# Kernel tuning notes

Measured on AMD Instinct MI355X. Metric: run time of the kernel, lower is better.

## Reference

```python
import jax, jax.numpy as jnp
import numpy as np

D = 1024      # in_features
H = 8         # heads per branch (head_num // 2)
DH = (D // 2) // H  # 64
OUT = 1024

def _split_heads(x, B, S):
    # [B, S, D/2] -> [B, H, S, DH]
    return x.reshape(B, S, H, DH).transpose(0, 2, 1, 3)

def _attn(q, k, v):
    # q,k,v: [B, H, S, DH]
    scores = jnp.einsum('bhqd,bhkd->bhqk', q, k) / jnp.sqrt(jnp.float32(DH))
    a = jax.nn.softmax(scores, axis=-1)
    return jnp.einsum('bhqk,bhkd->bhqd', a, v)

def setup_inputs() -> dict:
    key = jax.random.key(0)
    ks = jax.random.split(key, 16)
    B, S = 2, 2048
    d2 = D // 2
    sc = lambda fan_in: 1.0 / np.sqrt(fan_in)
    inp = {
        'f1': jax.random.normal(ks[0], (B, S, D), jnp.float32),
        'f2': jax.random.normal(ks[1], (B, S, D), jnp.float32),
    }
    names = ['qs', 'ks', 'vs', 'qc', 'kc', 'vc']
    for i, n in enumerate(names):
        inp['W' + n] = jax.random.uniform(ks[2 + i], (d2, D), jnp.float32, -sc(D), sc(D))
        inp['b' + n] = jax.random.uniform(ks[8 + i], (d2,), jnp.float32, -sc(D), sc(D))
    inp['Wo'] = jax.random.uniform(ks[14], (OUT, 2 * D), jnp.float32, -sc(2 * D), sc(2 * D))
    inp['bo'] = jax.random.uniform(ks[15], (OUT,), jnp.float32, -sc(2 * D), sc(2 * D))
    return inp

def reference(f1, f2, Wqs, bqs, Wks, bks, Wvs, bvs, Wqc, bqc, Wkc, bkc, Wvc, bvc, Wo, bo):
    B, S, _ = f1.shape
    lin = lambda x, W, b: jax.nn.relu(x @ W.T + b)
    qs = lin(f1, Wqs, bqs); ks_ = lin(f1, Wks, bks); vs = lin(f1, Wvs, bvs)
    qc = lin(f1, Wqc, bqc); kc = lin(f2, Wkc, bkc); vc = lin(f2, Wvc, bvc)
    ys = _attn(_split_heads(qs, B, S), _split_heads(ks_, B, S), _split_heads(vs, B, S))
    yc = _attn(_split_heads(qc, B, S), _split_heads(kc, B, S), _split_heads(vc, B, S))
    merge = lambda y: y.transpose(0, 2, 1, 3).reshape(B, S, D // 2)
    # reshape_to_batches followed by reshape_from_batches on vs/vc is identity
    y = jnp.concatenate([merge(ys), merge(yc), vs, vc], axis=-1)  # [B, S, 2D]
    return jax.nn.relu(y @ Wo.T + bo)
```

## Files before the change

### kernel.cpp

```cpp
#include <hip/hip_runtime.h>
#include <hip/hip_bf16.h>

using bf16 = __hip_bfloat16;
typedef __attribute__((ext_vector_type(8))) short bf16x8;
typedef __attribute__((ext_vector_type(4))) short s16x4;
typedef __attribute__((ext_vector_type(4))) float f32x4;
typedef __attribute__((ext_vector_type(16))) float f32x16;
typedef __attribute__((ext_vector_type(4))) unsigned int u32x4;

#define MTOT 4096

__device__ __forceinline__ f32x4 fzero() {
    f32x4 z = {0.f, 0.f, 0.f, 0.f};
    return z;
}
__device__ __forceinline__ f32x16 fzero16() {
    f32x16 z = {0.f,0.f,0.f,0.f,0.f,0.f,0.f,0.f,0.f,0.f,0.f,0.f,0.f,0.f,0.f,0.f};
    return z;
}

__device__ __forceinline__ f32x4 mfma16(bf16x8 a, bf16x8 b, f32x4 c) {
    return __builtin_amdgcn_mfma_f32_16x16x32_bf16(a, b, c, 0, 0, 0);
}
__device__ __forceinline__ f32x16 mfma32(bf16x8 a, bf16x8 b, f32x16 c) {
    return __builtin_amdgcn_mfma_f32_32x32x16_bf16(a, b, c, 0, 0, 0);
}

__device__ __forceinline__ float exp2_raw(float x) {
    float r;
    asm("v_exp_f32 %0, %1" : "=v"(r) : "v"(x));
    return r;
}

typedef const __attribute__((address_space(1))) unsigned int* gas_ptr;
typedef __attribute__((address_space(3))) unsigned int* las_ptr;
__device__ __forceinline__ void async_copy16(const bf16* g, bf16* l) {
    __builtin_amdgcn_global_load_lds((gas_ptr)(const void*)g, (las_ptr)(void*)l, 16, 0, 0);
}

__device__ __forceinline__ bf16x8 load8(const bf16* p) {
    return *(const bf16x8*)p;
}
__device__ __forceinline__ bf16x8 load8(const float* p) {
    float4 a = *(const float4*)p;
    float4 b = *(const float4*)(p + 4);
    bf16 t[8];
    t[0] = __float2bfloat16(a.x); t[1] = __float2bfloat16(a.y);
    t[2] = __float2bfloat16(a.z); t[3] = __float2bfloat16(a.w);
    t[4] = __float2bfloat16(b.x); t[5] = __float2bfloat16(b.y);
    t[6] = __float2bfloat16(b.z); t[7] = __float2bfloat16(b.w);
    return *(const bf16x8*)t;
}

__device__ __forceinline__ void store_out(bf16* C, size_t idx, float v) {
    C[idx] = __float2bfloat16(v);
}
__device__ __forceinline__ void store_out(float* C, size_t idx, float v) {
    C[idx] = v;
}
__device__ __forceinline__ short bf16_bits(float v) {
    return __builtin_bit_cast(short, __float2bfloat16(v));
}

__global__ void MultiHeadSelfCrossAttention_7834020348638_kernel(float* out, int n) {
    int i = blockIdx.x * blockDim.x + threadIdx.x;
    if (i < n) out[i] = 0.25f;
}

struct CvtArgs {
    const float* src[9];
    bf16* dst[9];
    int start8[10];
};
__global__ void cvt_kernel(CvtArgs a) {
    int t = blockIdx.x * blockDim.x + threadIdx.x;
    if (t >= a.start8[9]) return;
    int seg = 0;
#pragma unroll
    for (int s = 1; s < 9; s++) seg += (t >= a.start8[s]) ? 1 : 0;
    int off = t - a.start8[seg];
    *(bf16x8*)(a.dst[seg] + (size_t)off * 8) = load8(a.src[seg] + (size_t)off * 8);
}

template <int BM, int BN, typename TC>
__device__ __forceinline__ void gemm_fast(
    const bf16* __restrict__ A, int lda,
    const bf16* __restrict__ Bt, int ldb,
    const float* __restrict__ bias,
    TC* __restrict__ C, int ldc,
    int K, int m0, int n0, bf16* __restrict__ VTW)
{
    constexpr int MI  = BM / 32;
    constexpr int NI  = BN / 32;
    constexpr int ACH = BM * 64 / 8 / 256;
    constexpr int BCH = BN * 64 / 8 / 256;

    __shared__ bf16 As[BM * 64];
    __shared__ bf16 Bs[BN * 64];

    const int tid  = threadIdx.x;
    const int lane = tid & 63;
    const int l15  = lane & 15, quad = lane >> 4;
    const int wave = tid >> 6;
    const int wr   = wave >> 1, wc = wave & 1;

    f32x4 acc[MI][NI];
#pragma unroll
    for (int mi = 0; mi < MI; mi++)
#pragma unroll
        for (int ni = 0; ni < NI; ni++)
            acc[mi][ni] = fzero();

    for (int k0 = 0; k0 < K; k0 += 64) {
        __syncthreads();
#pragma unroll
        for (int i = 0; i < ACH; i++) {
            int idx = i * 256 + tid;
            int r   = idx >> 3;
            int sl  = (idx & 7) ^ (r & 7);
            async_copy16(A + (size_t)(m0 + r) * lda + k0 + sl * 8, &As[idx * 8]);
        }
#pragma unroll
        for (int i = 0; i < BCH; i++) {
            int idx = i * 256 + tid;
            int r   = idx >> 3;
            int sl  = (idx & 7) ^ (r & 7);
            async_copy16(Bt + (size_t)(n0 + r) * ldb + k0 + sl * 8, &Bs[idx * 8]);
        }
        __syncthreads();

#pragma unroll
        for (int ks = 0; ks < 2; ks++) {
            bf16x8 af[MI], bfr[NI];
#pragma unroll
            for (int mi = 0; mi < MI; mi++) {
                int row = wr * (BM / 2) + mi * 16 + l15;
                af[mi] = *(const bf16x8*)&As[row * 64 + (((ks * 4 + quad) ^ (row & 7)) * 8)];
            }
#pragma unroll
            for (int ni = 0; ni < NI; ni++) {
                int row = wc * (BN / 2) + ni * 16 + l15;
                bfr[ni] = *(const bf16x8*)&Bs[row * 64 + (((ks * 4 + quad) ^ (row & 7)) * 8)];
            }
#pragma unroll
            for (int mi = 0; mi < MI; mi++)
#pragma unroll
                for (int ni = 0; ni < NI; ni++)
                    acc[mi][ni] = mfma16(af[mi], bfr[ni], acc[mi][ni]);
        }
    }

#pragma unroll
    for (int ni = 0; ni < NI; ni++) {
        int col = n0 + wc * (BN / 2) + ni * 16 + l15;
        float bb = bias[col];
#pragma unroll
        for (int mi = 0; mi < MI; mi++) {
            float v0 = fmaxf(acc[mi][ni][0] + bb, 0.f);
            float v1 = fmaxf(acc[mi][ni][1] + bb, 0.f);
            float v2 = fmaxf(acc[mi][ni][2] + bb, 0.f);
            float v3 = fmaxf(acc[mi][ni][3] + bb, 0.f);
            int row0 = m0 + wr * (BM / 2) + mi * 16 + quad * 4;
            store_out(C, (size_t)(row0 + 0) * ldc + col, v0);
            store_out(C, (size_t)(row0 + 1) * ldc + col, v1);
            store_out(C, (size_t)(row0 + 2) * ldc + col, v2);
            store_out(C, (size_t)(row0 + 3) * ldc + col, v3);
            if (VTW) {
                int h = col >> 6, d = col & 63;
                int s = row0 & 2047, b2 = row0 >> 11;
                short tv[4] = {bf16_bits(v0), bf16_bits(v1), bf16_bits(v2), bf16_bits(v3)};
                *(s16x4*)&VTW[((size_t)(b2 * 8 + h)) * 64 * 2048 + (size_t)d * 2048 + s] =
                    *(const s16x4*)tv;
            }
        }
    }
}

template <int BN, typename TA, typename TB, typename TC>
__device__ __forceinline__ void gemm_reg(
    const TA* __restrict__ A, int lda,
    const TB* __restrict__ Bt, int ldb,
    const float* __restrict__ bias,
    TC* __restrict__ C, int ldc,
    int K, int m0, int n0)
{
    constexpr int NI  = BN / 32;
    constexpr int BCH = BN * 4 / 256;

    __shared__ bf16 As[128 * 32];
    __shared__ bf16 Bs[BN * 32];

    const int tid  = threadIdx.x;
    const int lane = tid & 63;
    const int l15  = lane & 15, quad = lane >> 4;
    const int wave = tid >> 6;
    const int wr   = wave >> 1, wc = wave & 1;

    f32x4 acc[4][NI];
#pragma unroll
    for (int mi = 0; mi < 4; mi++)
#pragma unroll
        for (int ni = 0; ni < NI; ni++)
            acc[mi][ni] = fzero();

    for (int k0 = 0; k0 < K; k0 += 32) {
        bf16x8 ra[2], rb[BCH];
#pragma unroll
        for (int i = 0; i < 2; i++) {
            int idx = i * 256 + tid;
            ra[i] = load8(A + (size_t)(m0 + (idx >> 2)) * lda + k0 + (idx & 3) * 8);
        }
#pragma unroll
        for (int i = 0; i < BCH; i++) {
            int idx = i * 256 + tid;
            rb[i] = load8(Bt + (size_t)(n0 + (idx >> 2)) * ldb + k0 + (idx & 3) * 8);
        }
        __syncthreads();
#pragma unroll
        for (int i = 0; i < 2; i++)
            *(bf16x8*)&As[(i * 256 + tid) * 8] = ra[i];
#pragma unroll
        for (int i = 0; i < BCH; i++)
            *(bf16x8*)&Bs[(i * 256 + tid) * 8] = rb[i];
        __syncthreads();

        bf16x8 af[4], bfr[NI];
#pragma unroll
        for (int mi = 0; mi < 4; mi++)
            af[mi] = *(const bf16x8*)&As[(wr * 64 + mi * 16 + l15) * 32 + quad * 8];
#pragma unroll
        for (int ni = 0; ni < NI; ni++)
            bfr[ni] = *(const bf16x8*)&Bs[(wc * (BN / 2) + ni * 16 + l15) * 32 + quad * 8];
#pragma unroll
        for (int mi = 0; mi < 4; mi++)
#pragma unroll
            for (int ni = 0; ni < NI; ni++)
                acc[mi][ni] = mfma16(af[mi], bfr[ni], acc[mi][ni]);
    }

#pragma unroll
    for (int ni = 0; ni < NI; ni++) {
        int col = n0 + wc * (BN / 2) + ni * 16 + l15;
        float bb = bias[col];
#pragma unroll
        for (int mi = 0; mi < 4; mi++) {
#pragma unroll
            for (int r = 0; r < 4; r++) {
                int row = m0 + wr * 64 + mi * 16 + quad * 4 + r;
                store_out(C, (size_t)row * ldc + col, fmaxf(acc[mi][ni][r] + bb, 0.f));
            }
        }
    }
}

__global__ __launch_bounds__(256, 4) void proj_fast(
    const bf16* __restrict__ F1, const bf16* __restrict__ F2,
    const bf16* __restrict__ Wb,
    const float* __restrict__ bqs, const float* __restrict__ bks,
    const float* __restrict__ bvs, const float* __restrict__ bqc,
    const float* __restrict__ bkc, const float* __restrict__ bvc,
    bf16* __restrict__ Y, bf16* Qs, bf16* Ks, bf16* Qc, bf16* Kc,
    bf16* __restrict__ VT)
{
    const int lid   = blockIdx.x;
    const int xcd   = lid & 7, slot = lid >> 3;
    const int panel = xcd * 24 + (slot >> 2);
    const int xb    = slot & 3;
    const int g     = panel >> 5, yb = panel & 31;
    const int m0 = yb * 128, n0 = xb * 128;

    const bf16* X; const float* bi; bf16* C; int ldc;
    switch (g) {
        case 0:  X = F1; bi = bqs; C = Qs;       ldc = 512;  break;
        case 1:  X = F1; bi = bks; C = Ks;       ldc = 512;  break;
        case 2:  X = F1; bi = bvs; C = Y + 1024; ldc = 2048; break;
        case 3:  X = F1; bi = bqc; C = Qc;       ldc = 512;  break;
        case 4:  X = F2; bi = bkc; C = Kc;       ldc = 512;  break;
        default: X = F2; bi = bvc; C = Y + 1536; ldc = 2048; break;
    }
    bf16* vtw = nullptr;
    if (VT && (g == 2 || g == 5))
        vtw = VT + (size_t)(g == 5 ? 2 * 8 * 64 * 2048 : 0);
    gemm_fast<128, 128, bf16>(X, 1024, Wb + (size_t)g * 512 * 1024, 1024, bi, C, ldc,
                              1024, m0, n0, vtw);
}

__global__ __launch_bounds__(256, 4) void out_fast(
    const bf16* __restrict__ Y, const bf16* __restrict__ WoB,
    const float* __restrict__ bo, float* __restrict__ out)
{
    const int lid   = blockIdx.x;
    const int xcd   = lid & 7, slot = lid >> 3;
    const int panel = xcd * 8 + (slot >> 4);
    const int xb    = slot & 15;
    gemm_fast<64, 64, float>(Y, 2048, WoB, 2048, bo, out, 1024, 2048,
                             panel * 64, xb * 64, nullptr);
}

__global__ void proj_reg(
    const float* __restrict__ f1, const float* __restrict__ f2,
    const float* __restrict__ Wqs, const float* __restrict__ bqs,
    const float* __restrict__ Wks, const float* __restrict__ bks,
    const float* __restrict__ Wvs, const float* __restrict__ bvs,
    const float* __restrict__ Wqc, const float* __restrict__ bqc,
    const float* __restrict__ Wkc, const float* __restrict__ bkc,
    const float* __restrict__ Wvc, const float* __restrict__ bvc,
    bf16* __restrict__ Y, bf16* Qs, bf16* Ks, bf16* Qc, bf16* Kc)
{
    const int g = blockIdx.z;
    const float *X, *W, *bi; bf16* C; int ldc;
    switch (g) {
        case 0:  X = f1; W = Wqs; bi = bqs; C = Qs;       ldc = 512;  break;
        case 1:  X = f1; W = Wks; bi = bks; C = Ks;       ldc = 512;  break;
        case 2:  X = f1; W = Wvs; bi = bvs; C = Y + 1024; ldc = 2048; break;
        case 3:  X = f1; W = Wqc; bi = bqc; C = Qc;       ldc = 512;  break;
        case 4:  X = f2; W = Wkc; bi = bkc; C = Kc;       ldc = 512;  break;
        default: X = f2; W = Wvc; bi = bvc; C = Y + 1536; ldc = 2048; break;
    }
    gemm_reg<128>(X, 1024, W, 1024, bi, C, ldc, 1024, blockIdx.y * 128, blockIdx.x * 128);
}

__global__ void out_reg(const bf16* __restrict__ Y, const float* __restrict__ Wo,
                        const float* __restrict__ bo, float* __restrict__ out)
{
    gemm_reg<64>(Y, 2048, Wo, 2048, bo, out, 1024, 2048, blockIdx.y * 128, blockIdx.x * 64);
}

__global__ __launch_bounds__(256, 4) void attn2_kernel(
    const bf16* __restrict__ Qsb, const bf16* __restrict__ Ksb,
    const bf16* __restrict__ Qcb, const bf16* __restrict__ Kcb,
    const bf16* __restrict__ VT, bf16* __restrict__ Y)
{
    __shared__ bf16 SMEM[4][64 * 64];

    const int tid  = threadIdx.x;
    const int lane = tid & 63;
    const int l31  = lane & 31;
    const int hi   = lane >> 5;
    const int wave = tid >> 6;

    const int lid   = blockIdx.x + 16 * blockIdx.y + 256 * blockIdx.z;
    const int xcd   = lid & 7, slot = lid >> 3;
    const int combo = xcd + 8 * (slot >> 4);
    const int qt    = slot & 15;
    const int bh    = combo & 15, br = combo >> 4;
    const int b = bh >> 3, h = bh & 7;

    const bf16* Qb = (br ? Qcb : Qsb) + (size_t)b * 2048 * 512 + h * 64;
    const bf16* Kb = (br ? Kcb : Ksb) + (size_t)b * 2048 * 512 + h * 64;
    const bf16* Vt = VT + ((size_t)((br * 2 + b) * 8 + h)) * 64 * 2048;
    bf16*       Ob = Y + (size_t)b * 2048 * 2048 + br * 512 + h * 64;
    const int q0 = qt * 128;

    bf16* QP = &SMEM[0][0];

#pragma unroll
    for (int i = 0; i < 4; i++) {
        int idx = i * 256 + tid;
        int r = idx >> 3, c0 = (idx & 7) * 8;
        *(bf16x8*)&QP[r * 72 + c0] = *(const bf16x8*)&Qb[(size_t)(q0 + r) * 512 + c0];
    }
    __syncthreads();

    bf16x8 qf[4];
#pragma unroll
    for (int kq = 0; kq < 4; kq++)
        qf[kq] = *(const bf16x8*)&QP[(wave * 32 + l31) * 72 + kq * 16 + hi * 8];
    __syncthreads();

#pragma unroll
    for (int i = 0; i < 2; i++) {
        int idx = i * 256 + tid;
        int r = idx >> 3, sl = (idx & 7) ^ (r & 7);
        async_copy16(Kb + (size_t)r * 512 + sl * 8, &SMEM[0][idx * 8]);
    }
#pragma unroll
    for (int i = 0; i < 2; i++) {
        int idx = i * 256 + tid;
        int r = idx >> 3, sl = (idx & 7) ^ (r & 7);
        async_copy16(Vt + (size_t)r * 2048 + sl * 8, &SMEM[1][idx * 8]);
    }
    __syncthreads();

    const short one_bits = (l31 == 0) ? (short)0x3F80 : (short)0;
    bf16x8 onesA;
#pragma unroll
    for (int j = 0; j < 8; j++) onesA[j] = one_bits;

    f32x16 o[2], ol;
    o[0] = fzero16(); o[1] = fzero16(); ol = fzero16();

    const float C1 = 0.18033688011112043f;
    const float C2 = -5.7707801635558535f;

    for (int jt = 0; jt < 32; jt++) {
        const int cur = jt & 1;
        const bf16* Kc = &SMEM[cur * 2][0];
        const bf16* Vc = &SMEM[cur * 2 + 1][0];

        if (jt < 31) {
            const size_t s0n = (size_t)(jt + 1) * 64;
            bf16* Kn = &SMEM[(cur ^ 1) * 2][0];
            bf16* Vn = &SMEM[(cur ^ 1) * 2 + 1][0];
#pragma unroll
            for (int i = 0; i < 2; i++) {
                int idx = i * 256 + tid;
                int r = idx >> 3, sl = (idx & 7) ^ (r & 7);
                async_copy16(Kb + (s0n + r) * 512 + sl * 8, &Kn[idx * 8]);
            }
#pragma unroll
            for (int i = 0; i < 2; i++) {
                int idx = i * 256 + tid;
                int r = idx >> 3, sl = (idx & 7) ^ (r & 7);
                async_copy16(Vt + (size_t)r * 2048 + s0n + sl * 8, &Vn[idx * 8]);
            }
        }

        f32x16 st[2];
        st[0] = fzero16(); st[1] = fzero16();
        __builtin_amdgcn_s_setprio(1);
#pragma unroll
        for (int t = 0; t < 2; t++)
#pragma unroll
            for (int kq = 0; kq < 4; kq++) {
                bf16x8 kf = *(const bf16x8*)&Kc[(t * 32 + l31) * 64
                               + (((kq * 2 + hi) ^ (l31 & 7)) * 8)];
                st[t] = mfma32(kf, qf[kq], st[t]);
            }
        __builtin_amdgcn_s_setprio(0);

        unsigned int pk[2][4][2];
#pragma unroll
        for (int t = 0; t < 2; t++)
#pragma unroll
            for (int g = 0; g < 4; g++) {
                float e0 = exp2_raw(fmaf(st[t][4 * g + 0], C1, C2));
                float e1 = exp2_raw(fmaf(st[t][4 * g + 1], C1, C2));
                float e2 = exp2_raw(fmaf(st[t][4 * g + 2], C1, C2));
                float e3 = exp2_raw(fmaf(st[t][4 * g + 3], C1, C2));
                asm("v_cvt_pk_bf16_f32 %0, %1, %2"
                    : "=v"(pk[t][g][0]) : "v"(e0), "v"(e1));
                asm("v_cvt_pk_bf16_f32 %0, %1, %2"
                    : "=v"(pk[t][g][1]) : "v"(e2), "v"(e3));
            }

        __builtin_amdgcn_s_setprio(1);
#pragma unroll
        for (int kb = 0; kb < 4; kb++) {
            const int t = kb >> 1, gb = (kb & 1) * 2;
            unsigned int u0 = pk[t][gb][0],     u1 = pk[t][gb][1];
            unsigned int v0 = pk[t][gb + 1][0], v1 = pk[t][gb + 1][1];
            asm("v_permlane32_swap_b32 %0, %1" : "+v"(u0), "+v"(v0));
            asm("v_permlane32_swap_b32 %0, %1" : "+v"(u1), "+v"(v1));
            u32x4 pw; pw.x = u0; pw.y = u1; pw.z = v0; pw.w = v1;
            bf16x8 pfrag = __builtin_bit_cast(bf16x8, pw);
#pragma unroll
            for (int dt = 0; dt < 2; dt++) {
                bf16x8 vf = *(const bf16x8*)&Vc[(dt * 32 + l31) * 64
                               + (((kb * 2 + hi) ^ (l31 & 7)) * 8)];
                o[dt] = mfma32(vf, pfrag, o[dt]);
            }
            ol = mfma32(onesA, pfrag, ol);
        }
        __builtin_amdgcn_s_setprio(0);

        __syncthreads();
    }

    const float linv = 1.0f / __shfl(ol[0], l31);
#pragma unroll
    for (int dt = 0; dt < 2; dt++)
#pragma unroll
        for (int r = 0; r < 16; r++) {
            int d = dt * 32 + (r & 3) + 8 * (r >> 2) + 4 * hi;
            QP[(wave * 32 + l31) * 72 + d] = __float2bfloat16(o[dt][r] * linv);
        }
    __syncthreads();
#pragma unroll
    for (int i = 0; i < 4; i++) {
        int idx = i * 256 + tid;
        int r = idx >> 3, c0 = (idx & 7) * 8;
        *(bf16x8*)&Ob[(size_t)(q0 + r) * 2048 + c0] = *(const bf16x8*)&QP[r * 72 + c0];
    }
}

__global__ __launch_bounds__(256, 4) void attn_kernel(
    const bf16* __restrict__ Qsb, const bf16* __restrict__ Ksb,
    const bf16* __restrict__ Qcb, const bf16* __restrict__ Kcb,
    bf16* __restrict__ Y)
{
    __shared__ bf16 QP[64 * 72];
    __shared__ bf16 Ksh[64 * 72];
    __shared__ bf16 Vsh[64 * 72];

    const int tid  = threadIdx.x;
    const int lane = tid & 63;
    const int l15  = lane & 15, quad = lane >> 4;
    const int wave = tid >> 6;
    const int qt = blockIdx.x, bh = blockIdx.y, br = blockIdx.z;
    const int b = bh >> 3, h = bh & 7;

    const bf16* Qb = (br ? Qcb : Qsb) + (size_t)b * 2048 * 512 + h * 64;
    const bf16* Kb = (br ? Kcb : Ksb) + (size_t)b * 2048 * 512 + h * 64;
    const bf16* Vb = Y + (size_t)b * 2048 * 2048 + 1024 + br * 512 + h * 64;
    bf16*       Ob = Y + (size_t)b * 2048 * 2048 +        br * 512 + h * 64;
    const int q0 = qt * 64;

#pragma unroll
    for (int i = 0; i < 2; i++) {
        int idx = i * 256 + tid;
        int r = idx >> 3, c0 = (idx & 7) * 8;
        *(bf16x8*)&QP[r * 72 + c0] = *(const bf16x8*)&Qb[(size_t)(q0 + r) * 512 + c0];
    }
    __syncthreads();

    bf16x8 qf[2];
#pragma unroll
    for (int ks = 0; ks < 2; ks++)
        qf[ks] = *(const bf16x8*)&QP[(wave * 16 + l15) * 72 + ks * 32 + quad * 8];

    const short one_bits = l15 == 0 ? (short)0x3F80 : (short)0;
    bf16x8 onesf;
#pragma unroll
    for (int j = 0; j < 8; j++) onesf[j] = one_bits;

    f32x4 o[4], o_l;
    o_l = fzero();
#pragma unroll
    for (int ni = 0; ni < 4; ni++) o[ni] = fzero();

    const int kr0 = tid >> 3, kc0 = (tid & 7) * 8;
    const int kr1 = (256 + tid) >> 3;

    bf16x8 kr[2], vr[2];
    kr[0] = *(const bf16x8*)&Kb[(size_t)kr0 * 512 + kc0];
    kr[1] = *(const bf16x8*)&Kb[(size_t)kr1 * 512 + kc0];
    vr[0] = *(const bf16x8*)&Vb[(size_t)lane * 2048 + (0 * 4 + wave) * 8];
    vr[1] = *(const bf16x8*)&Vb[(size_t)lane * 2048 + (1 * 4 + wave) * 8];

    for (int jt = 0; jt < 32; jt++) {
        __syncthreads();
        *(bf16x8*)&Ksh[kr0 * 72 + kc0] = kr[0];
        *(bf16x8*)&Ksh[kr1 * 72 + kc0] = kr[1];
#pragma unroll
        for (int i = 0; i < 2; i++) {
            int cg = i * 4 + wave;
            const bf16* e = (const bf16*)&vr[i];
#pragma unroll
            for (int j = 0; j < 8; j++)
                Vsh[(cg * 8 + j) * 72 + lane] = e[j];
        }
        __syncthreads();

        {
            const int s0n = (jt < 31) ? (jt + 1) * 64 : 31 * 64;
            kr[0] = *(const bf16x8*)&Kb[(size_t)(s0n + kr0) * 512 + kc0];
            kr[1] = *(const bf16x8*)&Kb[(size_t)(s0n + kr1) * 512 + kc0];
            vr[0] = *(const bf16x8*)&Vb[(size_t)(s0n + lane) * 2048 + (0 * 4 + wave) * 8];
            vr[1] = *(const bf16x8*)&Vb[(size_t)(s0n + lane) * 2048 + (1 * 4 + wave) * 8];
        }

        f32x4 s[4];
#pragma unroll
        for (int ni = 0; ni < 4; ni++) s[ni] = fzero();
#pragma unroll
        for (int ni = 0; ni < 4; ni++)
#pragma unroll
            for (int ks = 0; ks < 2; ks++) {
                bf16x8 kf = *(const bf16x8*)&Ksh[(ni * 16 + l15) * 72 + ks * 32 + quad * 8];
                s[ni] = mfma16(qf[ks], kf, s[ni]);
            }

#pragma unroll
        for (int ni = 0; ni < 4; ni++)
#pragma unroll
            for (int r = 0; r < 4; r++) {
                float p = __expf(s[ni][r] * 0.125f - 4.0f);
                QP[(wave * 16 + quad * 4 + r) * 72 + ni * 16 + l15] = __float2bfloat16(p);
            }

#pragma unroll
        for (int ks = 0; ks < 2; ks++) {
            bf16x8 pf = *(const bf16x8*)&QP[(wave * 16 + l15) * 72 + ks * 32 + quad * 8];
#pragma unroll
            for (int ni = 0; ni < 4; ni++) {
                bf16x8 vf = *(const bf16x8*)&Vsh[(ni * 16 + l15) * 72 + ks * 32 + quad * 8];
                o[ni] = mfma16(pf, vf, o[ni]);
            }
            o_l = mfma16(pf, onesf, o_l);
        }
    }

#pragma unroll
    for (int r = 0; r < 4; r++) {
        float lsum = __shfl(o_l[r], quad << 4);
        float inv = 1.f / lsum;
        int row = q0 + wave * 16 + quad * 4 + r;
#pragma unroll
        for (int ni = 0; ni < 4; ni++)
            Ob[(size_t)row * 2048 + ni * 16 + l15] = __float2bfloat16(o[ni][r] * inv);
    }
}

extern "C" void kernel_launch(void* const* d_in, const int* in_sizes, int n_in,
                              void* d_out, int out_size, void* d_ws, size_t ws_size,
                              hipStream_t stream) {
    const size_t out_bytes = (size_t)out_size * sizeof(float);
    const size_t ws_base = ((size_t)MTOT * 2048 + 4 * (size_t)MTOT * 512) * 2;
    const size_t ws_fast = ws_base + ((size_t)2 * MTOT * 1024 + 6 * 512 * 1024 + 1024 * 2048) * 2;
    const size_t vt_elems = (size_t)2 * 2 * 8 * 64 * 2048;
    const size_t ws_fast2 = ws_fast + vt_elems * 2;

    if (n_in != 16) { hipMemsetAsync(d_out, 0x43, out_bytes, stream); return; }
    if (ws_size < ws_base) { hipMemsetAsync(d_out, 0x41, out_bytes, stream); return; }

    const float* f1  = (const float*)d_in[0];
    const float* f2  = (const float*)d_in[1];
    const float* Wqs = (const float*)d_in[2];  const float* bqs = (const float*)d_in[3];
    const float* Wks = (const float*)d_in[4];  const float* bks = (const float*)d_in[5];
    const float* Wvs = (const float*)d_in[6];  const float* bvs = (const float*)d_in[7];
    const float* Wqc = (const float*)d_in[8];  const float* bqc = (const float*)d_in[9];
    const float* Wkc = (const float*)d_in[10]; const float* bkc = (const float*)d_in[11];
    const float* Wvc = (const float*)d_in[12]; const float* bvc = (const float*)d_in[13];
    const float* Wo  = (const float*)d_in[14]; const float* bo  = (const float*)d_in[15];

    bf16* Y  = (bf16*)d_ws;
    bf16* Qs = Y  + (size_t)MTOT * 2048;
    bf16* Ks = Qs + (size_t)MTOT * 512;
    bf16* Qc = Ks + (size_t)MTOT * 512;
    bf16* Kc = Qc + (size_t)MTOT * 512;
    float* out = (float*)d_out;

    if (ws_size >= ws_fast) {
        bf16* F1  = Kc + (size_t)MTOT * 512;
        bf16* F2  = F1 + (size_t)MTOT * 1024;
        bf16* Wb  = F2 + (size_t)MTOT * 1024;
        bf16* WoB = Wb + (size_t)6 * 512 * 1024;
        bf16* VT  = WoB + (size_t)1024 * 2048;
        const bool fast2 = (ws_size >= ws_fast2);

        CvtArgs ca;
        ca.src[0] = f1;  ca.dst[0] = F1;
        ca.src[1] = f2;  ca.dst[1] = F2;
        const float* ws_[6] = {Wqs, Wks, Wvs, Wqc, Wkc, Wvc};
        for (int i = 0; i < 6; i++) {
            ca.src[2 + i] = ws_[i];
            ca.dst[2 + i] = Wb + (size_t)i * 512 * 1024;
        }
        ca.src[8] = Wo; ca.dst[8] = WoB;
        int acc8 = 0;
        const int sizes8[9] = {MTOT * 1024 / 8, MTOT * 1024 / 8,
                               512 * 1024 / 8, 512 * 1024 / 8, 512 * 1024 / 8,
                               512 * 1024 / 8, 512 * 1024 / 8, 512 * 1024 / 8,
                               1024 * 2048 / 8};
        for (int i = 0; i < 9; i++) { ca.start8[i] = acc8; acc8 += sizes8[i]; }
        ca.start8[9] = acc8;

        cvt_kernel<<<dim3((acc8 + 255) / 256), 256, 0, stream>>>(ca);
        proj_fast<<<768, 256, 0, stream>>>(
            F1, F2, Wb, bqs, bks, bvs, bqc, bkc, bvc, Y, Qs, Ks, Qc, Kc,
            fast2 ? VT : nullptr);
        if (fast2) {
            attn2_kernel<<<dim3(16, 16, 2), 256, 0, stream>>>(Qs, Ks, Qc, Kc, VT, Y);
        } else {
            attn_kernel<<<dim3(32, 16, 2), 256, 0, stream>>>(Qs, Ks, Qc, Kc, Y);
        }
        out_fast<<<1024, 256, 0, stream>>>(Y, WoB, bo, out);
    } else {
        proj_reg<<<dim3(4, 32, 6), 256, 0, stream>>>(
            f1, f2, Wqs, bqs, Wks, bks, Wvs, bvs, Wqc, bqc, Wkc, bkc, Wvc, bvc,
            Y, Qs, Ks, Qc, Kc);
        attn_kernel<<<dim3(32, 16, 2), 256, 0, stream>>>(Qs, Ks, Qc, Kc, Y);
        out_reg<<<dim3(16, 32), 256, 0, stream>>>(Y, Wo, bo, out);
    }
}
```

Baseline: 221.4 us.

## Split-K output GEMM with 128x128 tiles and stage V-transpose writes through LDS

The output projection switches from 64x64 tiles over K=2048 to two K-halves computed with 128x128 tiles into fp32 partial buffers. A separate combine kernel then sums the halves and applies bias and ReLU. The V-transposed write in the projection epilogue is now staged through a swizzled shared-memory tile so global stores are contiguous 16-byte rows instead of scattered 8-byte writes. This aims for better MFMA data reuse and store coalescing, at the cost of an extra kernel launch and 32 MB of fp32 partial traffic.

```diff
diff --git a/kernel.cpp b/kernel.cpp
--- a/kernel.cpp
+++ b/kernel.cpp
@@ -82,7 +82,7 @@
     *(bf16x8*)(a.dst[seg] + (size_t)off * 8) = load8(a.src[seg] + (size_t)off * 8);
 }
 
-template <int BM, int BN, typename TC>
+template <int BM, int BN, bool RAW, typename TC>
 __device__ __forceinline__ void gemm_fast(
     const bf16* __restrict__ A, int lda,
     const bf16* __restrict__ Bt, int ldb,
@@ -95,8 +95,9 @@
     constexpr int ACH = BM * 64 / 8 / 256;
     constexpr int BCH = BN * 64 / 8 / 256;
 
-    __shared__ bf16 As[BM * 64];
-    __shared__ bf16 Bs[BN * 64];
+    __shared__ bf16 SM[BM * 64 + BN * 64];
+    bf16* As = SM;
+    bf16* Bs = SM + BM * 64;
 
     const int tid  = threadIdx.x;
     const int lane = tid & 63;
@@ -150,27 +151,55 @@
         }
     }
 
+    const bool dovt = (VTW != nullptr);
+    if constexpr (BM == 128 && BN == 128) {
+        if (dovt) __syncthreads();
+    }
+
 #pragma unroll
     for (int ni = 0; ni < NI; ni++) {
         int col = n0 + wc * (BN / 2) + ni * 16 + l15;
-        float bb = bias[col];
+        float bb = 0.f;
+        if constexpr (!RAW) bb = bias[col];
 #pragma unroll
         for (int mi = 0; mi < MI; mi++) {
-            float v0 = fmaxf(acc[mi][ni][0] + bb, 0.f);
-            float v1 = fmaxf(acc[mi][ni][1] + bb, 0.f);
-            float v2 = fmaxf(acc[mi][ni][2] + bb, 0.f);
-            float v3 = fmaxf(acc[mi][ni][3] + bb, 0.f);
+            float v0 = acc[mi][ni][0] + bb;
+            float v1 = acc[mi][ni][1] + bb;
+            float v2 = acc[mi][ni][2] + bb;
+            float v3 = acc[mi][ni][3] + bb;
+            if constexpr (!RAW) {
+                v0 = fmaxf(v0, 0.f); v1 = fmaxf(v1, 0.f);
+                v2 = fmaxf(v2, 0.f); v3 = fmaxf(v3, 0.f);
+            }
             int row0 = m0 + wr * (BM / 2) + mi * 16 + quad * 4;
             store_out(C, (size_t)(row0 + 0) * ldc + col, v0);
             store_out(C, (size_t)(row0 + 1) * ldc + col, v1);
             store_out(C, (size_t)(row0 + 2) * ldc + col, v2);
             store_out(C, (size_t)(row0 + 3) * ldc + col, v3);
-            if (VTW) {
-                int h = col >> 6, d = col & 63;
-                int s = row0 & 2047, b2 = row0 >> 11;
-                short tv[4] = {bf16_bits(v0), bf16_bits(v1), bf16_bits(v2), bf16_bits(v3)};
-                *(s16x4*)&VTW[((size_t)(b2 * 8 + h)) * 64 * 2048 + (size_t)d * 2048 + s] =
-                    *(const s16x4*)tv;
+            if constexpr (BM == 128 && BN == 128) {
+                if (dovt) {
+                    int cl = wc * 64 + ni * 16 + l15;
+                    int rl0 = wr * 64 + mi * 16 + quad * 4;
+                    int rX = rl0 ^ ((cl & 7) << 3);
+                    short tv[4] = {bf16_bits(v0), bf16_bits(v1),
+                                   bf16_bits(v2), bf16_bits(v3)};
+                    *(s16x4*)&SM[cl * 128 + rX] = *(const s16x4*)tv;
+                }
+            }
+        }
+    }
+
+    if constexpr (BM == 128 && BN == 128) {
+        if (dovt) {
+            __syncthreads();
+#pragma unroll
+            for (int i = 0; i < 8; i++) {
+                int idx = i * 256 + tid;
+                int d2 = idx >> 4, j = idx & 15;
+                bf16x8 vv = *(const bf16x8*)&SM[d2 * 128 + ((j * 8) ^ ((d2 & 7) << 3))];
+                int h = (n0 + d2) >> 6, din = (n0 + d2) & 63;
+                int s = (m0 & 2047) + j * 8, b2 = m0 >> 11;
+                *(bf16x8*)&VTW[((size_t)(b2 * 8 + h) * 64 + din) * 2048 + s] = vv;
             }
         }
     }
@@ -281,8 +310,8 @@
     bf16* vtw = nullptr;
     if (VT && (g == 2 || g == 5))
         vtw = VT + (size_t)(g == 5 ? 2 * 8 * 64 * 2048 : 0);
-    gemm_fast<128, 128, bf16>(X, 1024, Wb + (size_t)g * 512 * 1024, 1024, bi, C, ldc,
-                              1024, m0, n0, vtw);
+    gemm_fast<128, 128, false, bf16>(X, 1024, Wb + (size_t)g * 512 * 1024, 1024, bi,
+                                     C, ldc, 1024, m0, n0, vtw);
 }
 
 __global__ __launch_bounds__(256, 4) void out_fast(
@@ -293,8 +322,40 @@
     const int xcd   = lid & 7, slot = lid >> 3;
     const int panel = xcd * 8 + (slot >> 4);
     const int xb    = slot & 15;
-    gemm_fast<64, 64, float>(Y, 2048, WoB, 2048, bo, out, 1024, 2048,
-                             panel * 64, xb * 64, nullptr);
+    gemm_fast<64, 64, false, float>(Y, 2048, WoB, 2048, bo, out, 1024, 2048,
+                                    panel * 64, xb * 64, nullptr);
+}
+
+__global__ __launch_bounds__(256, 4) void out_split(
+    const bf16* __restrict__ Y, const bf16* __restrict__ WoB,
+    float* __restrict__ PK)
+{
+    const int lid   = blockIdx.x;
+    const int xcd   = lid & 7, slot = lid >> 3;
+    const int panel = xcd * 8 + (slot >> 3);
+    const int xb    = slot & 7;
+    const int yb    = panel & 31, kh = panel >> 5;
+    gemm_fast<128, 128, true, float>(
+        Y + (size_t)kh * 1024, 2048, WoB + (size_t)kh * 1024, 2048, nullptr,
+        PK + (size_t)kh * MTOT * 1024, 1024, 1024, yb * 128, xb * 128, nullptr);
+}
+
+__global__ void out_combine(const float* __restrict__ PK,
+                            const float* __restrict__ bo,
+                            float* __restrict__ out)
+{
+    size_t i4 = (size_t)blockIdx.x * 256 + threadIdx.x;
+    if (i4 >= (size_t)MTOT * 1024 / 4) return;
+    float4 a = ((const float4*)PK)[i4];
+    float4 b = ((const float4*)(PK + (size_t)MTOT * 1024))[i4];
+    int col4 = (int)((i4 * 4) & 1023);
+    float4 bb = *(const float4*)&bo[col4];
+    float4 r;
+    r.x = fmaxf(a.x + b.x + bb.x, 0.f);
+    r.y = fmaxf(a.y + b.y + bb.y, 0.f);
+    r.z = fmaxf(a.z + b.z + bb.z, 0.f);
+    r.w = fmaxf(a.w + b.w + bb.w, 0.f);
+    ((float4*)out)[i4] = r;
 }
 
 __global__ void proj_reg(
@@ -610,6 +671,7 @@
     const size_t ws_fast = ws_base + ((size_t)2 * MTOT * 1024 + 6 * 512 * 1024 + 1024 * 2048) * 2;
     const size_t vt_elems = (size_t)2 * 2 * 8 * 64 * 2048;
     const size_t ws_fast2 = ws_fast + vt_elems * 2;
+    const size_t ws_split = ws_fast2 + (size_t)2 * MTOT * 1024 * 4;
 
     if (n_in != 16) { hipMemsetAsync(d_out, 0x43, out_bytes, stream); return; }
     if (ws_size < ws_base) { hipMemsetAsync(d_out, 0x41, out_bytes, stream); return; }
@@ -637,7 +699,9 @@
         bf16* Wb  = F2 + (size_t)MTOT * 1024;
         bf16* WoB = Wb + (size_t)6 * 512 * 1024;
         bf16* VT  = WoB + (size_t)1024 * 2048;
+        float* PK = (float*)(VT + vt_elems);
         const bool fast2 = (ws_size >= ws_fast2);
+        const bool fast3 = (ws_size >= ws_split);
 
         CvtArgs ca;
         ca.src[0] = f1;  ca.dst[0] = F1;
@@ -665,7 +729,12 @@
         } else {
             attn_kernel<<<dim3(32, 16, 2), 256, 0, stream>>>(Qs, Ks, Qc, Kc, Y);
         }
-        out_fast<<<1024, 256, 0, stream>>>(Y, WoB, bo, out);
+        if (fast3) {
+            out_split<<<512, 256, 0, stream>>>(Y, WoB, PK);
+            out_combine<<<dim3(MTOT * 1024 / 4 / 256), 256, 0, stream>>>(PK, bo, out);
+        } else {
+            out_fast<<<1024, 256, 0, stream>>>(Y, WoB, bo, out);
+        }
     } else {
         proj_reg<<<dim3(4, 32, 6), 256, 0, stream>>>(
             f1, f2, Wqs, bqs, Wks, bks, Wvs, bvs, Wqc, bqc, Wkc, bkc, Wvc, bvc,
```

Result: no change. 223.2 us (+0.8%).
